# Kernel optimization log

Hardware: AMD Instinct MI355X
Metric: run time of the kernel (lower is better)

Reference implementation:

```python
import jax, jax.numpy as jnp
import numpy as np

F = 64          # n_features
H = F * F       # n_hidden = 4096
P = 4           # proj_size
T = 8192        # timesteps


def _proj_lstm_cell_zero_state(x, W_ih, W_hh, b_ih, b_hh, W_hr):
    """One PyTorch proj-LSTM layer applied per-timestep with zero initial
    (h, c). x: [T, in_dim] -> [T, P].  With h0=0, W_hh contributes 0 and
    f*c_prev vanishes."""
    h0 = jnp.zeros((x.shape[0], W_hh.shape[1]), x.dtype)
    gates = x @ W_ih.T + h0 @ W_hh.T + b_ih + b_hh          # [T, 4H]
    i, f, g, o = jnp.split(gates, 4, axis=-1)               # PyTorch gate order
    c = jax.nn.sigmoid(i) * jnp.tanh(g)                     # f*c0 = 0
    h = jax.nn.sigmoid(o) * jnp.tanh(c)                     # [T, H]
    return h @ W_hr.T                                       # [T, P]


def setup_inputs() -> dict:
    key = jax.random.key(0)
    ks = jax.random.split(key, 17)
    s = 0.05
    d = {"x": jax.random.normal(ks[0], (T, F), jnp.float32)}
    shapes = {
        "W_ih_0": (4 * H, F), "W_hh_0": (4 * H, P), "b_ih_0": (4 * H,),
        "b_hh_0": (4 * H,), "W_hr_0": (P, H),
        "W_ih_1": (4 * H, P), "W_hh_1": (4 * H, P), "b_ih_1": (4 * H,),
        "b_hh_1": (4 * H,), "W_hr_1": (P, H),
        "W_ih_2": (4 * H, P), "W_hh_2": (4 * H, P), "b_ih_2": (4 * H,),
        "b_hh_2": (4 * H,), "W_hr_2": (P, H),
    }
    for i, (name, shp) in enumerate(shapes.items()):
        d[name] = s * jax.random.normal(ks[i + 1], shp, jnp.float32)
    return d


def reference(x,
              W_ih_0, W_hh_0, b_ih_0, b_hh_0, W_hr_0,
              W_ih_1, W_hh_1, b_ih_1, b_hh_1, W_hr_1,
              W_ih_2, W_hh_2, b_ih_2, b_hh_2, W_hr_2):
    # study(): inputs.split(1, dim=0) feeds each timestep as a fresh length-1
    # sequence with zero initial state, so timesteps are independent ->
    # vectorize over T instead of the per-step Python loop.
    h = _proj_lstm_cell_zero_state(x, W_ih_0, W_hh_0, b_ih_0, b_hh_0, W_hr_0)
    h = _proj_lstm_cell_zero_state(h, W_ih_1, W_hh_1, b_ih_1, b_hh_1, W_hr_1)
    h = _proj_lstm_cell_zero_state(h, W_ih_2, W_hh_2, b_ih_2, b_hh_2, W_hr_2)
    return h  # [T, P]
```

## Files before the change

kernel.cpp:

```cpp
#include <hip/hip_runtime.h>

#define TSTEPS 8192
#define HDIM 4096
#define PDIM 4
#define KDIM 64

typedef unsigned short u16;
typedef __attribute__((ext_vector_type(8))) short short8;
typedef __attribute__((ext_vector_type(4))) float f32x4;

#define S1 -1.44269504089f
#define S2 -2.88539008177f

#if __has_builtin(__builtin_amdgcn_exp2f)
#define EXP2(x) __builtin_amdgcn_exp2f(x)
#else
#define EXP2(x) exp2f(x)
#endif
__device__ __forceinline__ float rcpf(float x) { return __builtin_amdgcn_rcpf(x); }

__device__ __forceinline__ void gload16(const void* g, void* l) {
  __builtin_amdgcn_global_load_lds((const __attribute__((address_space(1))) unsigned int*)g,
                                   (__attribute__((address_space(3))) unsigned int*)l,
                                   16, 0, 0);
}

__device__ __forceinline__ u16 bf16_rne(float f) {
  unsigned u = __float_as_uint(f);
  u += 0x7FFF + ((u >> 16) & 1);
  return (u16)(u >> 16);
}
__device__ __forceinline__ void hilo(float v, u16& h, u16& l) {
  h = bf16_rne(v);
  l = bf16_rne(v - __uint_as_float((unsigned)h << 16));
}

#define WS_Y0   0
#define WS_Y1   32768
#define WS_BSC  65536
#define WS_C1   77824
#define WS_C2   159744
#define WS_XHI  241664
#define WS_XLO  503808
#define WS_WHI  765952
#define WS_WLO  1159168
#define WS_PP   1552384

__global__ void prep_kernel(const float* __restrict__ x,
                            const float* __restrict__ Wih0, const float* __restrict__ bih0,
                            const float* __restrict__ bhh0,
                            const float* __restrict__ Wih1, const float* __restrict__ bih1,
                            const float* __restrict__ bhh1, const float* __restrict__ Whr1,
                            const float* __restrict__ Wih2, const float* __restrict__ bih2,
                            const float* __restrict__ bhh2, const float* __restrict__ Whr2,
                            float* __restrict__ ws) {
  const int i = blockIdx.x * 256 + threadIdx.x;
  u16* xhi = (u16*)(ws + WS_XHI);
  u16* xlo = (u16*)(ws + WS_XLO);
  u16* whi = (u16*)(ws + WS_WHI);
  u16* wlo = (u16*)(ws + WS_WLO);

  if (i < 131072) {
    float4 v = *(const float4*)&x[i * 4];
    float val[4] = {v.x, v.y, v.z, v.w};
    u16 h[4], l[4];
#pragma unroll
    for (int e = 0; e < 4; ++e) hilo(val[e], h[e], l[e]);
    *(ushort4*)&xhi[i * 4] = make_ushort4(h[0], h[1], h[2], h[3]);
    *(ushort4*)&xlo[i * 4] = make_ushort4(l[0], l[1], l[2], l[3]);
  } else if (i < 327680) {
    int f = i - 131072;
    int el4 = f * 4;
    int r = el4 >> 6;
    int k4 = el4 & 63;
    int gate = r >> 12, jr = r & 4095;
    int src = (gate == 0) ? jr : (gate + 1) * HDIM + jr;
    float sc = (gate == 1) ? S2 : S1;
    float4 v = *(const float4*)&Wih0[(size_t)src * KDIM + k4];
    float val[4] = {sc * v.x, sc * v.y, sc * v.z, sc * v.w};
    u16 h[4], l[4];
#pragma unroll
    for (int e = 0; e < 4; ++e) hilo(val[e], h[e], l[e]);
    *(ushort4*)&whi[r * KDIM + k4] = make_ushort4(h[0], h[1], h[2], h[3]);
    *(ushort4*)&wlo[r * KDIM + k4] = make_ushort4(l[0], l[1], l[2], l[3]);
  } else if (i < 339968) {
    int f = i - 327680;
    int g = f >> 12, j = f & 4095;
    int src = (g == 0) ? j : (g + 1) * HDIM + j;
    float sc = (g == 1) ? S2 : S1;
    ws[WS_BSC + f] = sc * (bih0[src] + bhh0[src]);
  } else if (i < 348160) {
    int f = i - 339968;
    const float* Wih = (f < 4096) ? Wih1 : Wih2;
    const float* bih = (f < 4096) ? bih1 : bih2;
    const float* bhh = (f < 4096) ? bhh1 : bhh2;
    const float* Whr = (f < 4096) ? Whr1 : Whr2;
    float* c = ws + ((f < 4096) ? WS_C1 : WS_C2);
    int j = f & 4095;
    float4 wi = *(const float4*)&Wih[(size_t)j * 4];
    float4 wg = *(const float4*)&Wih[(size_t)(2 * HDIM + j) * 4];
    float4 wo = *(const float4*)&Wih[(size_t)(3 * HDIM + j) * 4];
    float* cb = c + j * 20;
    *(float4*)(cb + 0)  = make_float4(S1 * wi.x, S1 * wi.y, S1 * wi.z, S1 * wi.w);
    *(float4*)(cb + 4)  = make_float4(S2 * wg.x, S2 * wg.y, S2 * wg.z, S2 * wg.w);
    *(float4*)(cb + 8)  = make_float4(S1 * wo.x, S1 * wo.y, S1 * wo.z, S1 * wo.w);
    *(float4*)(cb + 12) = make_float4(S1 * (bih[j] + bhh[j]),
                                      S2 * (bih[2 * HDIM + j] + bhh[2 * HDIM + j]),
                                      S1 * (bih[3 * HDIM + j] + bhh[3 * HDIM + j]), 0.f);
    *(float4*)(cb + 16) = make_float4(Whr[j], Whr[HDIM + j], Whr[2 * HDIM + j], Whr[3 * HDIM + j]);
  }
}

__global__ __launch_bounds__(256, 2)
void lstm_layer0_mfma(const u16* __restrict__ xhi, const u16* __restrict__ xlo,
                      const u16* __restrict__ whi, const u16* __restrict__ wlo,
                      const float* __restrict__ bsc, const float* __restrict__ Whr,
                      float* __restrict__ pp) {
  __shared__ __align__(16) char smem[65536];
  u16* lx_hi = (u16*)smem;
  u16* lw_hi = (u16*)(smem + 16384);
  u16* lw_lo = (u16*)(smem + 40960);
  float* hsh = (float*)smem;

  const int tid = threadIdx.x;
  const int w = tid >> 6, lane = tid & 63;
  const int m = lane & 15, q = lane >> 4;
  const int jb = blockIdx.x & 63, tb = blockIdx.x >> 6;
  const int j0 = jb * 64;
  const int t0 = tb * 128;

  const int r8 = lane >> 3;
  const int swo = ((lane & 7) ^ r8) * 8;
#pragma unroll
  for (int ui = 0; ui < 16; ++ui) {
    const int u = w * 16 + ui;
    const u16* g;
    char* l;
    if (u < 16) {
      g = xhi + (size_t)(t0 + u * 8 + r8) * 64 + swo;
      l = smem + u * 1024;
    } else if (u < 40) {
      int uu = u - 16;
      g = whi + (size_t)((uu >> 3) * HDIM + j0 + (uu & 7) * 8 + r8) * 64 + swo;
      l = smem + 16384 + uu * 1024;
    } else {
      int uu = u - 40;
      g = wlo + (size_t)((uu >> 3) * HDIM + j0 + (uu & 7) * 8 + r8) * 64 + swo;
      l = smem + 40960 + uu * 1024;
    }
    gload16(g, l);
  }

  f32x4 acc[2][4][3];
#pragma unroll
  for (int ts = 0; ts < 2; ++ts)
#pragma unroll
    for (int js = 0; js < 4; ++js)
#pragma unroll
      for (int g = 0; g < 3; ++g) acc[ts][js][g] = (f32x4){0.f, 0.f, 0.f, 0.f};

  short8 al[2][2];
#pragma unroll
  for (int kc = 0; kc < 2; ++kc)
#pragma unroll
    for (int ts = 0; ts < 2; ++ts)
      al[kc][ts] = *(const short8*)&xlo[(size_t)(t0 + w * 32 + ts * 16 + m) * KDIM + kc * 32 + q * 8];

  __syncthreads();

#pragma unroll
  for (int kc = 0; kc < 2; ++kc) {
    const int cs = ((kc * 4 + q) ^ (m & 7)) * 8;
    short8 ah[2];
#pragma unroll
    for (int ts = 0; ts < 2; ++ts)
      ah[ts] = *(const short8*)&lx_hi[(w * 32 + ts * 16 + m) * 64 + cs];
#pragma unroll
    for (int js = 0; js < 4; ++js) {
#pragma unroll
      for (int g = 0; g < 3; ++g) {
        const int roff = (g * 64 + js * 16 + m) * 64 + cs;
        short8 bh = *(const short8*)&lw_hi[roff];
        short8 bl = *(const short8*)&lw_lo[roff];
#pragma unroll
        for (int ts = 0; ts < 2; ++ts) {
          acc[ts][js][g] = __builtin_amdgcn_mfma_f32_16x16x32_bf16(ah[ts], bh, acc[ts][js][g], 0, 0, 0);
          acc[ts][js][g] = __builtin_amdgcn_mfma_f32_16x16x32_bf16(al[kc][ts], bh, acc[ts][js][g], 0, 0, 0);
          acc[ts][js][g] = __builtin_amdgcn_mfma_f32_16x16x32_bf16(ah[ts], bl, acc[ts][js][g], 0, 0, 0);
        }
      }
    }
  }

  float hreg[2][4][4];
#pragma unroll
  for (int js = 0; js < 4; ++js) {
    const int j = j0 + js * 16 + m;
    float bi = bsc[j];
    float bg = bsc[HDIM + j];
    float bo = bsc[2 * HDIM + j];
#pragma unroll
    for (int ts = 0; ts < 2; ++ts) {
#pragma unroll
      for (int r = 0; r < 4; ++r) {
        float ea = EXP2(acc[ts][js][0][r] + bi);
        float eb = EXP2(acc[ts][js][1][r] + bg);
        float c = (1.0f - eb) * rcpf((1.0f + ea) * (1.0f + eb));
        float ec = EXP2(acc[ts][js][2][r] + bo);
        float ed = EXP2(S2 * c);
        hreg[ts][js][r] = (1.0f - ed) * rcpf((1.0f + ec) * (1.0f + ed));
      }
    }
  }
  __syncthreads();

#pragma unroll
  for (int js = 0; js < 4; ++js)
#pragma unroll
    for (int ts = 0; ts < 2; ++ts)
#pragma unroll
      for (int r = 0; r < 4; ++r)
        hsh[(w * 32 + ts * 16 + q * 4 + r) * 68 + js * 16 + m] = hreg[ts][js][r];
  __syncthreads();

  const int tl = tid & 127;
  const int p0 = (tid >> 7) * 2;
  float s0 = 0.f, s1 = 0.f;
#pragma unroll
  for (int cch = 0; cch < 8; ++cch) {
    const float* wp0 = Whr + (size_t)p0 * HDIM + j0 + cch * 8;
    const float* wp1 = Whr + (size_t)(p0 + 1) * HDIM + j0 + cch * 8;
    float4 w0a = *(const float4*)wp0, w0b = *(const float4*)(wp0 + 4);
    float4 w1a = *(const float4*)wp1, w1b = *(const float4*)(wp1 + 4);
    float4 ha = *(const float4*)&hsh[tl * 68 + cch * 8];
    float4 hb = *(const float4*)&hsh[tl * 68 + cch * 8 + 4];
    float wa[8] = {w0a.x, w0a.y, w0a.z, w0a.w, w0b.x, w0b.y, w0b.z, w0b.w};
    float wb[8] = {w1a.x, w1a.y, w1a.z, w1a.w, w1b.x, w1b.y, w1b.z, w1b.w};
    float hv[8] = {ha.x, ha.y, ha.z, ha.w, hb.x, hb.y, hb.z, hb.w};
#pragma unroll
    for (int e = 0; e < 8; ++e) {
      s0 = fmaf(hv[e], wa[e], s0);
      s1 = fmaf(hv[e], wb[e], s1);
    }
  }
  const int tg = tb * 128 + tl;
  float2 st = {s0, s1};
  *(float2*)&pp[((size_t)jb * TSTEPS + tg) * PDIM + p0] = st;
}

__global__ void reduce64(const float* __restrict__ pp, float* __restrict__ y) {
  const int i = blockIdx.x * 256 + threadIdx.x;
  float s = 0.f;
#pragma unroll 16
  for (int k = 0; k < 64; ++k) s += pp[(size_t)k * (TSTEPS * PDIM) + i];
  y[i] = s;
}

__global__ __launch_bounds__(256, 4)
void lstm_small(const float* __restrict__ xin, const float* __restrict__ cpk,
                float* __restrict__ pp) {
  __shared__ __align__(16) float rec[1280];
  const int tid = threadIdx.x;
  const int tc = blockIdx.x >> 6;
  const int jsp = blockIdx.x & 63;
  const int j0 = jsp * 64;

  for (int i = tid; i < 320; i += 256)
    ((float4*)rec)[i] = ((const float4*)(cpk + (size_t)j0 * 20))[i];

  const int ta = tc * 512 + tid;
  const int tb2 = ta + 256;
  float4 xa = ((const float4*)xin)[ta];
  float4 xb = ((const float4*)xin)[tb2];
  float a0 = 0.f, a1 = 0.f, a2 = 0.f, a3 = 0.f;
  float b0 = 0.f, b1 = 0.f, b2 = 0.f, b3 = 0.f;
  __syncthreads();

#pragma unroll 4
  for (int jj = 0; jj < 64; ++jj) {
    const float* cb = rec + jj * 20;
    float4 wi = *(const float4*)(cb + 0);
    float4 wg = *(const float4*)(cb + 4);
    float4 wo = *(const float4*)(cb + 8);
    float4 bb = *(const float4*)(cb + 12);
    float4 wr = *(const float4*)(cb + 16);
    float gi = bb.x, gg = bb.y, go = bb.z;
    gi = fmaf(xa.x, wi.x, gi); gi = fmaf(xa.y, wi.y, gi);
    gi = fmaf(xa.z, wi.z, gi); gi = fmaf(xa.w, wi.w, gi);
    gg = fmaf(xa.x, wg.x, gg); gg = fmaf(xa.y, wg.y, gg);
    gg = fmaf(xa.z, wg.z, gg); gg = fmaf(xa.w, wg.w, gg);
    go = fmaf(xa.x, wo.x, go); go = fmaf(xa.y, wo.y, go);
    go = fmaf(xa.z, wo.z, go); go = fmaf(xa.w, wo.w, go);
    float ea = EXP2(gi), eb = EXP2(gg);
    float c = (1.0f - eb) * rcpf((1.0f + ea) * (1.0f + eb));
    float ec = EXP2(go), ed = EXP2(S2 * c);
    float h = (1.0f - ed) * rcpf((1.0f + ec) * (1.0f + ed));
    a0 = fmaf(h, wr.x, a0); a1 = fmaf(h, wr.y, a1);
    a2 = fmaf(h, wr.z, a2); a3 = fmaf(h, wr.w, a3);
    gi = bb.x; gg = bb.y; go = bb.z;
    gi = fmaf(xb.x, wi.x, gi); gi = fmaf(xb.y, wi.y, gi);
    gi = fmaf(xb.z, wi.z, gi); gi = fmaf(xb.w, wi.w, gi);
    gg = fmaf(xb.x, wg.x, gg); gg = fmaf(xb.y, wg.y, gg);
    gg = fmaf(xb.z, wg.z, gg); gg = fmaf(xb.w, wg.w, gg);
    go = fmaf(xb.x, wo.x, go); go = fmaf(xb.y, wo.y, go);
    go = fmaf(xb.z, wo.z, go); go = fmaf(xb.w, wo.w, go);
    ea = EXP2(gi); eb = EXP2(gg);
    c = (1.0f - eb) * rcpf((1.0f + ea) * (1.0f + eb));
    ec = EXP2(go); ed = EXP2(S2 * c);
    h = (1.0f - ed) * rcpf((1.0f + ec) * (1.0f + ed));
    b0 = fmaf(h, wr.x, b0); b1 = fmaf(h, wr.y, b1);
    b2 = fmaf(h, wr.z, b2); b3 = fmaf(h, wr.w, b3);
  }

  ((float4*)pp)[(size_t)jsp * TSTEPS + ta]  = make_float4(a0, a1, a2, a3);
  ((float4*)pp)[(size_t)jsp * TSTEPS + tb2] = make_float4(b0, b1, b2, b3);
}

extern "C" void kernel_launch(void* const* d_in, const int* in_sizes, int n_in,
                              void* d_out, int out_size, void* d_ws, size_t ws_size,
                              hipStream_t stream) {
  const float* x    = (const float*)d_in[0];
  const float* Wih0 = (const float*)d_in[1];
  const float* bih0 = (const float*)d_in[3];
  const float* bhh0 = (const float*)d_in[4];
  const float* Whr0 = (const float*)d_in[5];
  const float* Wih1 = (const float*)d_in[6];
  const float* bih1 = (const float*)d_in[8];
  const float* bhh1 = (const float*)d_in[9];
  const float* Whr1 = (const float*)d_in[10];
  const float* Wih2 = (const float*)d_in[11];
  const float* bih2 = (const float*)d_in[13];
  const float* bhh2 = (const float*)d_in[14];
  const float* Whr2 = (const float*)d_in[15];
  float* out = (float*)d_out;
  float* ws = (float*)d_ws;
  float* pp = ws + WS_PP;

  prep_kernel<<<dim3(1360), dim3(256), 0, stream>>>(
      x, Wih0, bih0, bhh0, Wih1, bih1, bhh1, Whr1, Wih2, bih2, bhh2, Whr2, ws);

  lstm_layer0_mfma<<<dim3(4096), dim3(256), 0, stream>>>(
      (const u16*)(ws + WS_XHI), (const u16*)(ws + WS_XLO),
      (const u16*)(ws + WS_WHI), (const u16*)(ws + WS_WLO),
      ws + WS_BSC, Whr0, pp);
  reduce64<<<dim3(128), dim3(256), 0, stream>>>(pp, ws + WS_Y0);

  lstm_small<<<dim3(1024), dim3(256), 0, stream>>>(ws + WS_Y0, ws + WS_C1, pp);
  reduce64<<<dim3(128), dim3(256), 0, stream>>>(pp, ws + WS_Y1);

  lstm_small<<<dim3(1024), dim3(256), 0, stream>>>(ws + WS_Y1, ws + WS_C2, pp);
  reduce64<<<dim3(128), dim3(256), 0, stream>>>(pp, out);
}
```

Measured before the change: 238.4 us.

## Reuse layer-0 weight tiles across two time tiles and shuffle-reduce the projection

The layer-0 MFMA kernel now handles 256 timesteps per block instead of 128. Weight hi/lo tiles stay resident in LDS, and the next x tile is prefetched into LDS while the activations and projection of the first tile run. The projection now uses register-resident Whr and a 16-lane shuffle reduction instead of an LDS round trip of h. Separately, lstm_small drops from two timesteps per thread to one, doubles its grid and raises its occupancy hint. The aim is to halve weight-tile global traffic, shorten the epilogue, and give the small layers more parallelism, at the cost of more registers and shuffles in layer 0.

```diff
diff --git a/kernel.cpp b/kernel.cpp
--- a/kernel.cpp
+++ b/kernel.cpp
@@ -117,135 +117,153 @@
                       const float* __restrict__ bsc, const float* __restrict__ Whr,
                       float* __restrict__ pp) {
   __shared__ __align__(16) char smem[65536];
-  u16* lx_hi = (u16*)smem;
-  u16* lw_hi = (u16*)(smem + 16384);
-  u16* lw_lo = (u16*)(smem + 40960);
-  float* hsh = (float*)smem;
+  u16* lw_hi = (u16*)smem;
+  u16* lw_lo = (u16*)(smem + 24576);
+  u16* lx    = (u16*)(smem + 49152);
 
   const int tid = threadIdx.x;
   const int w = tid >> 6, lane = tid & 63;
   const int m = lane & 15, q = lane >> 4;
-  const int jb = blockIdx.x & 63, tb = blockIdx.x >> 6;
+  const int jb = blockIdx.x & 63, tbb = blockIdx.x >> 6;
   const int j0 = jb * 64;
-  const int t0 = tb * 128;
+  const int t0 = tbb * 256;
 
   const int r8 = lane >> 3;
   const int swo = ((lane & 7) ^ r8) * 8;
+
 #pragma unroll
   for (int ui = 0; ui < 16; ++ui) {
     const int u = w * 16 + ui;
     const u16* g;
     char* l;
-    if (u < 16) {
-      g = xhi + (size_t)(t0 + u * 8 + r8) * 64 + swo;
+    if (u < 24) {
+      g = whi + (size_t)((u >> 3) * HDIM + j0 + (u & 7) * 8 + r8) * 64 + swo;
       l = smem + u * 1024;
-    } else if (u < 40) {
-      int uu = u - 16;
-      g = whi + (size_t)((uu >> 3) * HDIM + j0 + (uu & 7) * 8 + r8) * 64 + swo;
-      l = smem + 16384 + uu * 1024;
+    } else if (u < 48) {
+      int uu = u - 24;
+      g = wlo + (size_t)((uu >> 3) * HDIM + j0 + (uu & 7) * 8 + r8) * 64 + swo;
+      l = smem + 24576 + uu * 1024;
     } else {
-      int uu = u - 40;
-      g = wlo + (size_t)((uu >> 3) * HDIM + j0 + (uu & 7) * 8 + r8) * 64 + swo;
-      l = smem + 40960 + uu * 1024;
+      int uu = u - 48;
+      g = xhi + (size_t)(t0 + uu * 8 + r8) * 64 + swo;
+      l = smem + 49152 + uu * 1024;
     }
     gload16(g, l);
   }
 
+  float whr_v[4][4];
+#pragma unroll
+  for (int p = 0; p < 4; ++p)
+#pragma unroll
+    for (int js = 0; js < 4; ++js)
+      whr_v[p][js] = Whr[(size_t)p * HDIM + j0 + js * 16 + m];
+  float biv[4], bgv[4], bov[4];
+#pragma unroll
+  for (int js = 0; js < 4; ++js) {
+    const int j = j0 + js * 16 + m;
+    biv[js] = bsc[j];
+    bgv[js] = bsc[HDIM + j];
+    bov[js] = bsc[2 * HDIM + j];
+  }
+
   f32x4 acc[2][4][3];
-#pragma unroll
-  for (int ts = 0; ts < 2; ++ts)
-#pragma unroll
-    for (int js = 0; js < 4; ++js)
-#pragma unroll
-      for (int g = 0; g < 3; ++g) acc[ts][js][g] = (f32x4){0.f, 0.f, 0.f, 0.f};
-
   short8 al[2][2];
-#pragma unroll
-  for (int kc = 0; kc < 2; ++kc)
+
+  auto zero_acc = [&]() {
 #pragma unroll
     for (int ts = 0; ts < 2; ++ts)
-      al[kc][ts] = *(const short8*)&xlo[(size_t)(t0 + w * 32 + ts * 16 + m) * KDIM + kc * 32 + q * 8];
-
-  __syncthreads();
-
-#pragma unroll
-  for (int kc = 0; kc < 2; ++kc) {
-    const int cs = ((kc * 4 + q) ^ (m & 7)) * 8;
-    short8 ah[2];
-#pragma unroll
-    for (int ts = 0; ts < 2; ++ts)
-      ah[ts] = *(const short8*)&lx_hi[(w * 32 + ts * 16 + m) * 64 + cs];
-#pragma unroll
-    for (int js = 0; js < 4; ++js) {
-#pragma unroll
-      for (int g = 0; g < 3; ++g) {
-        const int roff = (g * 64 + js * 16 + m) * 64 + cs;
-        short8 bh = *(const short8*)&lw_hi[roff];
-        short8 bl = *(const short8*)&lw_lo[roff];
-#pragma unroll
-        for (int ts = 0; ts < 2; ++ts) {
-          acc[ts][js][g] = __builtin_amdgcn_mfma_f32_16x16x32_bf16(ah[ts], bh, acc[ts][js][g], 0, 0, 0);
-          acc[ts][js][g] = __builtin_amdgcn_mfma_f32_16x16x32_bf16(al[kc][ts], bh, acc[ts][js][g], 0, 0, 0);
-          acc[ts][js][g] = __builtin_amdgcn_mfma_f32_16x16x32_bf16(ah[ts], bl, acc[ts][js][g], 0, 0, 0);
+#pragma unroll
+      for (int js = 0; js < 4; ++js)
+#pragma unroll
+        for (int g = 0; g < 3; ++g) acc[ts][js][g] = (f32x4){0.f, 0.f, 0.f, 0.f};
+  };
+  auto load_al = [&](int tt) {
+#pragma unroll
+    for (int kc = 0; kc < 2; ++kc)
+#pragma unroll
+      for (int ts = 0; ts < 2; ++ts)
+        al[kc][ts] = *(const short8*)&xlo[(size_t)(t0 + tt * 128 + w * 32 + ts * 16 + m) * KDIM + kc * 32 + q * 8];
+  };
+  auto compute = [&]() {
+#pragma unroll
+    for (int kc = 0; kc < 2; ++kc) {
+      const int cs = ((kc * 4 + q) ^ (m & 7)) * 8;
+      short8 ah[2];
+#pragma unroll
+      for (int ts = 0; ts < 2; ++ts)
+        ah[ts] = *(const short8*)&lx[(w * 32 + ts * 16 + m) * 64 + cs];
+#pragma unroll
+      for (int js = 0; js < 4; ++js) {
+#pragma unroll
+        for (int g = 0; g < 3; ++g) {
+          const int roff = (g * 64 + js * 16 + m) * 64 + cs;
+          short8 bh = *(const short8*)&lw_hi[roff];
+          short8 bl = *(const short8*)&lw_lo[roff];
+#pragma unroll
+          for (int ts = 0; ts < 2; ++ts) {
+            acc[ts][js][g] = __builtin_amdgcn_mfma_f32_16x16x32_bf16(ah[ts], bh, acc[ts][js][g], 0, 0, 0);
+            acc[ts][js][g] = __builtin_amdgcn_mfma_f32_16x16x32_bf16(al[kc][ts], bh, acc[ts][js][g], 0, 0, 0);
+            acc[ts][js][g] = __builtin_amdgcn_mfma_f32_16x16x32_bf16(ah[ts], bl, acc[ts][js][g], 0, 0, 0);
+          }
         }
       }
     }
-  }
-
-  float hreg[2][4][4];
-#pragma unroll
-  for (int js = 0; js < 4; ++js) {
-    const int j = j0 + js * 16 + m;
-    float bi = bsc[j];
-    float bg = bsc[HDIM + j];
-    float bo = bsc[2 * HDIM + j];
-#pragma unroll
-    for (int ts = 0; ts < 2; ++ts) {
-#pragma unroll
-      for (int r = 0; r < 4; ++r) {
-        float ea = EXP2(acc[ts][js][0][r] + bi);
-        float eb = EXP2(acc[ts][js][1][r] + bg);
-        float c = (1.0f - eb) * rcpf((1.0f + ea) * (1.0f + eb));
-        float ec = EXP2(acc[ts][js][2][r] + bo);
-        float ed = EXP2(S2 * c);
-        hreg[ts][js][r] = (1.0f - ed) * rcpf((1.0f + ec) * (1.0f + ed));
+  };
+  auto act_proj = [&](int tt) {
+    float hreg[2][4][4];
+#pragma unroll
+    for (int js = 0; js < 4; ++js) {
+#pragma unroll
+      for (int ts = 0; ts < 2; ++ts) {
+#pragma unroll
+        for (int r = 0; r < 4; ++r) {
+          float ea = EXP2(acc[ts][js][0][r] + biv[js]);
+          float eb = EXP2(acc[ts][js][1][r] + bgv[js]);
+          float c = (1.0f - eb) * rcpf((1.0f + ea) * (1.0f + eb));
+          float ec = EXP2(acc[ts][js][2][r] + bov[js]);
+          float ed = EXP2(S2 * c);
+          hreg[ts][js][r] = (1.0f - ed) * rcpf((1.0f + ec) * (1.0f + ed));
+        }
       }
     }
-  }
+#pragma unroll
+    for (int ts = 0; ts < 2; ++ts) {
+#pragma unroll
+      for (int r = 0; r < 4; ++r) {
+        float pv[4];
+#pragma unroll
+        for (int p = 0; p < 4; ++p) {
+          float s = 0.f;
+#pragma unroll
+          for (int js = 0; js < 4; ++js) s = fmaf(hreg[ts][js][r], whr_v[p][js], s);
+#pragma unroll
+          for (int ofs = 1; ofs < 16; ofs <<= 1) s += __shfl_xor(s, ofs, 16);
+          pv[p] = s;
+        }
+        if (m == 0) {
+          const int t = t0 + tt * 128 + w * 32 + ts * 16 + q * 4 + r;
+          *(float4*)&pp[((size_t)jb * TSTEPS + t) * PDIM] = make_float4(pv[0], pv[1], pv[2], pv[3]);
+        }
+      }
+    }
+  };
+
+  load_al(0);
+  zero_acc();
   __syncthreads();
-
-#pragma unroll
-  for (int js = 0; js < 4; ++js)
-#pragma unroll
-    for (int ts = 0; ts < 2; ++ts)
-#pragma unroll
-      for (int r = 0; r < 4; ++r)
-        hsh[(w * 32 + ts * 16 + q * 4 + r) * 68 + js * 16 + m] = hreg[ts][js][r];
+  compute();
   __syncthreads();
-
-  const int tl = tid & 127;
-  const int p0 = (tid >> 7) * 2;
-  float s0 = 0.f, s1 = 0.f;
-#pragma unroll
-  for (int cch = 0; cch < 8; ++cch) {
-    const float* wp0 = Whr + (size_t)p0 * HDIM + j0 + cch * 8;
-    const float* wp1 = Whr + (size_t)(p0 + 1) * HDIM + j0 + cch * 8;
-    float4 w0a = *(const float4*)wp0, w0b = *(const float4*)(wp0 + 4);
-    float4 w1a = *(const float4*)wp1, w1b = *(const float4*)(wp1 + 4);
-    float4 ha = *(const float4*)&hsh[tl * 68 + cch * 8];
-    float4 hb = *(const float4*)&hsh[tl * 68 + cch * 8 + 4];
-    float wa[8] = {w0a.x, w0a.y, w0a.z, w0a.w, w0b.x, w0b.y, w0b.z, w0b.w};
-    float wb[8] = {w1a.x, w1a.y, w1a.z, w1a.w, w1b.x, w1b.y, w1b.z, w1b.w};
-    float hv[8] = {ha.x, ha.y, ha.z, ha.w, hb.x, hb.y, hb.z, hb.w};
-#pragma unroll
-    for (int e = 0; e < 8; ++e) {
-      s0 = fmaf(hv[e], wa[e], s0);
-      s1 = fmaf(hv[e], wb[e], s1);
-    }
-  }
-  const int tg = tb * 128 + tl;
-  float2 st = {s0, s1};
-  *(float2*)&pp[((size_t)jb * TSTEPS + tg) * PDIM + p0] = st;
+#pragma unroll
+  for (int ui = 0; ui < 4; ++ui) {
+    const int u = w * 4 + ui;
+    gload16(xhi + (size_t)(t0 + 128 + u * 8 + r8) * 64 + swo, smem + 49152 + u * 1024);
+  }
+  load_al(1);
+  act_proj(0);
+  zero_acc();
+  __syncthreads();
+  compute();
+  act_proj(1);
 }
 
 __global__ void reduce64(const float* __restrict__ pp, float* __restrict__ y) {
@@ -256,7 +274,7 @@
   y[i] = s;
 }
 
-__global__ __launch_bounds__(256, 4)
+__global__ __launch_bounds__(256, 8)
 void lstm_small(const float* __restrict__ xin, const float* __restrict__ cpk,
                 float* __restrict__ pp) {
   __shared__ __align__(16) float rec[1280];
@@ -268,15 +286,12 @@
   for (int i = tid; i < 320; i += 256)
     ((float4*)rec)[i] = ((const float4*)(cpk + (size_t)j0 * 20))[i];
 
-  const int ta = tc * 512 + tid;
-  const int tb2 = ta + 256;
-  float4 xa = ((const float4*)xin)[ta];
-  float4 xb = ((const float4*)xin)[tb2];
-  float a0 = 0.f, a1 = 0.f, a2 = 0.f, a3 = 0.f;
-  float b0 = 0.f, b1 = 0.f, b2 = 0.f, b3 = 0.f;
+  const int t = tc * 256 + tid;
+  float4 xv = ((const float4*)xin)[t];
+  float o0 = 0.f, o1 = 0.f, o2 = 0.f, o3 = 0.f;
   __syncthreads();
 
-#pragma unroll 4
+#pragma unroll 8
   for (int jj = 0; jj < 64; ++jj) {
     const float* cb = rec + jj * 20;
     float4 wi = *(const float4*)(cb + 0);
@@ -285,35 +300,21 @@
     float4 bb = *(const float4*)(cb + 12);
     float4 wr = *(const float4*)(cb + 16);
     float gi = bb.x, gg = bb.y, go = bb.z;
-    gi = fmaf(xa.x, wi.x, gi); gi = fmaf(xa.y, wi.y, gi);
-    gi = fmaf(xa.z, wi.z, gi); gi = fmaf(xa.w, wi.w, gi);
-    gg = fmaf(xa.x, wg.x, gg); gg = fmaf(xa.y, wg.y, gg);
-    gg = fmaf(xa.z, wg.z, gg); gg = fmaf(xa.w, wg.w, gg);
-    go = fmaf(xa.x, wo.x, go); go = fmaf(xa.y, wo.y, go);
-    go = fmaf(xa.z, wo.z, go); go = fmaf(xa.w, wo.w, go);
+    gi = fmaf(xv.x, wi.x, gi); gi = fmaf(xv.y, wi.y, gi);
+    gi = fmaf(xv.z, wi.z, gi); gi = fmaf(xv.w, wi.w, gi);
+    gg = fmaf(xv.x, wg.x, gg); gg = fmaf(xv.y, wg.y, gg);
+    gg = fmaf(xv.z, wg.z, gg); gg = fmaf(xv.w, wg.w, gg);
+    go = fmaf(xv.x, wo.x, go); go = fmaf(xv.y, wo.y, go);
+    go = fmaf(xv.z, wo.z, go); go = fmaf(xv.w, wo.w, go);
     float ea = EXP2(gi), eb = EXP2(gg);
     float c = (1.0f - eb) * rcpf((1.0f + ea) * (1.0f + eb));
     float ec = EXP2(go), ed = EXP2(S2 * c);
     float h = (1.0f - ed) * rcpf((1.0f + ec) * (1.0f + ed));
-    a0 = fmaf(h, wr.x, a0); a1 = fmaf(h, wr.y, a1);
-    a2 = fmaf(h, wr.z, a2); a3 = fmaf(h, wr.w, a3);
-    gi = bb.x; gg = bb.y; go = bb.z;
-    gi = fmaf(xb.x, wi.x, gi); gi = fmaf(xb.y, wi.y, gi);
-    gi = fmaf(xb.z, wi.z, gi); gi = fmaf(xb.w, wi.w, gi);
-    gg = fmaf(xb.x, wg.x, gg); gg = fmaf(xb.y, wg.y, gg);
-    gg = fmaf(xb.z, wg.z, gg); gg = fmaf(xb.w, wg.w, gg);
-    go = fmaf(xb.x, wo.x, go); go = fmaf(xb.y, wo.y, go);
-    go = fmaf(xb.z, wo.z, go); go = fmaf(xb.w, wo.w, go);
-    ea = EXP2(gi); eb = EXP2(gg);
-    c = (1.0f - eb) * rcpf((1.0f + ea) * (1.0f + eb));
-    ec = EXP2(go); ed = EXP2(S2 * c);
-    h = (1.0f - ed) * rcpf((1.0f + ec) * (1.0f + ed));
-    b0 = fmaf(h, wr.x, b0); b1 = fmaf(h, wr.y, b1);
-    b2 = fmaf(h, wr.z, b2); b3 = fmaf(h, wr.w, b3);
-  }
-
-  ((float4*)pp)[(size_t)jsp * TSTEPS + ta]  = make_float4(a0, a1, a2, a3);
-  ((float4*)pp)[(size_t)jsp * TSTEPS + tb2] = make_float4(b0, b1, b2, b3);
+    o0 = fmaf(h, wr.x, o0); o1 = fmaf(h, wr.y, o1);
+    o2 = fmaf(h, wr.z, o2); o3 = fmaf(h, wr.w, o3);
+  }
+
+  ((float4*)pp)[(size_t)jsp * TSTEPS + t] = make_float4(o0, o1, o2, o3);
 }
 
 extern "C" void kernel_launch(void* const* d_in, const int* in_sizes, int n_in,
@@ -339,15 +340,15 @@
   prep_kernel<<<dim3(1360), dim3(256), 0, stream>>>(
       x, Wih0, bih0, bhh0, Wih1, bih1, bhh1, Whr1, Wih2, bih2, bhh2, Whr2, ws);
 
-  lstm_layer0_mfma<<<dim3(4096), dim3(256), 0, stream>>>(
+  lstm_layer0_mfma<<<dim3(2048), dim3(256), 0, stream>>>(
       (const u16*)(ws + WS_XHI), (const u16*)(ws + WS_XLO),
       (const u16*)(ws + WS_WHI), (const u16*)(ws + WS_WLO),
       ws + WS_BSC, Whr0, pp);
   reduce64<<<dim3(128), dim3(256), 0, stream>>>(pp, ws + WS_Y0);
 
-  lstm_small<<<dim3(1024), dim3(256), 0, stream>>>(ws + WS_Y0, ws + WS_C1, pp);
+  lstm_small<<<dim3(2048), dim3(256), 0, stream>>>(ws + WS_Y0, ws + WS_C1, pp);
   reduce64<<<dim3(128), dim3(256), 0, stream>>>(pp, ws + WS_Y1);
 
-  lstm_small<<<dim3(1024), dim3(256), 0, stream>>>(ws + WS_Y1, ws + WS_C2, pp);
+  lstm_small<<<dim3(2048), dim3(256), 0, stream>>>(ws + WS_Y1, ws + WS_C2, pp);
   reduce64<<<dim3(128), dim3(256), 0, stream>>>(pp, out);
 }
```

Measured after the change: 232.8 us. 1.02x faster.

## Retile layer-0 MFMA kernel, fuse projection via shuffles, use Padé tanh

Applied to the files above, without the earlier changes.

The layer-0 MFMA kernel now handles 64 timesteps per block instead of 128, and each wave covers half of the hidden tile. The x hi/lo fragments load straight from global into registers, and the LDS footprint shrinks so three blocks can fit per CU. The W_hr projection is done in registers with cross-lane shuffle reductions plus a small LDS merge, which replaces the staged h tile and the separate dot-product pass. tanh(c) is replaced everywhere by a rational Padé approximation that saves one exp2. This relies on c staying in (-1,1), and it adds some approximation error and more shuffle work in exchange.

```diff
diff --git a/kernel.cpp b/kernel.cpp
--- a/kernel.cpp
+++ b/kernel.cpp
@@ -18,6 +18,13 @@
 #define EXP2(x) exp2f(x)
 #endif
 __device__ __forceinline__ float rcpf(float x) { return __builtin_amdgcn_rcpf(x); }
+
+__device__ __forceinline__ float h_merge(float c, float ec) {
+  float c2 = c * c;
+  float num = c * fmaf(c2, 10.0f, 105.0f);
+  float den = fmaf(c2, 45.0f, 105.0f) + c2 * c2;
+  return num * rcpf(den * (1.0f + ec));
+}
 
 __device__ __forceinline__ void gload16(const void* g, void* l) {
   __builtin_amdgcn_global_load_lds((const __attribute__((address_space(1))) unsigned int*)g,
@@ -111,141 +118,122 @@
   }
 }
 
-__global__ __launch_bounds__(256, 2)
+__global__ __launch_bounds__(256, 3)
 void lstm_layer0_mfma(const u16* __restrict__ xhi, const u16* __restrict__ xlo,
                       const u16* __restrict__ whi, const u16* __restrict__ wlo,
                       const float* __restrict__ bsc, const float* __restrict__ Whr,
                       float* __restrict__ pp) {
-  __shared__ __align__(16) char smem[65536];
-  u16* lx_hi = (u16*)smem;
-  u16* lw_hi = (u16*)(smem + 16384);
-  u16* lw_lo = (u16*)(smem + 40960);
-  float* hsh = (float*)smem;
+  __shared__ __align__(16) char smem[51200];
+  u16* lw_hi = (u16*)smem;
+  u16* lw_lo = (u16*)(smem + 24576);
+  float* red = (float*)(smem + 49152);
 
   const int tid = threadIdx.x;
   const int w = tid >> 6, lane = tid & 63;
   const int m = lane & 15, q = lane >> 4;
-  const int jb = blockIdx.x & 63, tb = blockIdx.x >> 6;
+  const int th = w & 1, jh = w >> 1;
+  const int jb = blockIdx.x & 63, tbb = blockIdx.x >> 6;
   const int j0 = jb * 64;
-  const int t0 = tb * 128;
-
-  const int r8 = lane >> 3;
-  const int swo = ((lane & 7) ^ r8) * 8;
-#pragma unroll
-  for (int ui = 0; ui < 16; ++ui) {
-    const int u = w * 16 + ui;
+  const int t0 = tbb * 64;
+
+  const int r8_ = lane >> 3;
+  const int swo = ((lane & 7) ^ r8_) * 8;
+
+#pragma unroll
+  for (int ui = 0; ui < 12; ++ui) {
+    const int u = w * 12 + ui;
     const u16* g;
-    char* l;
-    if (u < 16) {
-      g = xhi + (size_t)(t0 + u * 8 + r8) * 64 + swo;
-      l = smem + u * 1024;
-    } else if (u < 40) {
-      int uu = u - 16;
-      g = whi + (size_t)((uu >> 3) * HDIM + j0 + (uu & 7) * 8 + r8) * 64 + swo;
-      l = smem + 16384 + uu * 1024;
+    if (u < 24) {
+      int row = u * 8 + r8_;
+      g = whi + (size_t)((row >> 6) * HDIM + j0 + (row & 63)) * 64 + swo;
     } else {
-      int uu = u - 40;
-      g = wlo + (size_t)((uu >> 3) * HDIM + j0 + (uu & 7) * 8 + r8) * 64 + swo;
-      l = smem + 40960 + uu * 1024;
+      int row = (u - 24) * 8 + r8_;
+      g = wlo + (size_t)((row >> 6) * HDIM + j0 + (row & 63)) * 64 + swo;
     }
-    gload16(g, l);
-  }
-
-  f32x4 acc[2][4][3];
+    gload16(g, smem + u * 1024);
+  }
+
+  short8 ah[2][2], al[2][2];
+#pragma unroll
+  for (int kc = 0; kc < 2; ++kc)
+#pragma unroll
+    for (int ts = 0; ts < 2; ++ts) {
+      size_t ax = (size_t)(t0 + th * 32 + ts * 16 + m) * KDIM + kc * 32 + q * 8;
+      ah[kc][ts] = *(const short8*)&xhi[ax];
+      al[kc][ts] = *(const short8*)&xlo[ax];
+    }
+
+  float whr_v[4][2], biv[2], bgv[2], bov[2];
+#pragma unroll
+  for (int js = 0; js < 2; ++js) {
+    const int j = j0 + jh * 32 + js * 16 + m;
+#pragma unroll
+    for (int p = 0; p < 4; ++p) whr_v[p][js] = Whr[(size_t)p * HDIM + j];
+    biv[js] = bsc[j];
+    bgv[js] = bsc[HDIM + j];
+    bov[js] = bsc[2 * HDIM + j];
+  }
+
+  f32x4 acc[2][2][3];
 #pragma unroll
   for (int ts = 0; ts < 2; ++ts)
 #pragma unroll
-    for (int js = 0; js < 4; ++js)
+    for (int js = 0; js < 2; ++js)
 #pragma unroll
       for (int g = 0; g < 3; ++g) acc[ts][js][g] = (f32x4){0.f, 0.f, 0.f, 0.f};
-
-  short8 al[2][2];
-#pragma unroll
-  for (int kc = 0; kc < 2; ++kc)
-#pragma unroll
-    for (int ts = 0; ts < 2; ++ts)
-      al[kc][ts] = *(const short8*)&xlo[(size_t)(t0 + w * 32 + ts * 16 + m) * KDIM + kc * 32 + q * 8];
 
   __syncthreads();
 
 #pragma unroll
   for (int kc = 0; kc < 2; ++kc) {
     const int cs = ((kc * 4 + q) ^ (m & 7)) * 8;
-    short8 ah[2];
-#pragma unroll
-    for (int ts = 0; ts < 2; ++ts)
-      ah[ts] = *(const short8*)&lx_hi[(w * 32 + ts * 16 + m) * 64 + cs];
-#pragma unroll
-    for (int js = 0; js < 4; ++js) {
+#pragma unroll
+    for (int js = 0; js < 2; ++js) {
 #pragma unroll
       for (int g = 0; g < 3; ++g) {
-        const int roff = (g * 64 + js * 16 + m) * 64 + cs;
+        const int roff = (g * 64 + jh * 32 + js * 16 + m) * 64 + cs;
         short8 bh = *(const short8*)&lw_hi[roff];
         short8 bl = *(const short8*)&lw_lo[roff];
 #pragma unroll
         for (int ts = 0; ts < 2; ++ts) {
-          acc[ts][js][g] = __builtin_amdgcn_mfma_f32_16x16x32_bf16(ah[ts], bh, acc[ts][js][g], 0, 0, 0);
+          acc[ts][js][g] = __builtin_amdgcn_mfma_f32_16x16x32_bf16(ah[kc][ts], bh, acc[ts][js][g], 0, 0, 0);
           acc[ts][js][g] = __builtin_amdgcn_mfma_f32_16x16x32_bf16(al[kc][ts], bh, acc[ts][js][g], 0, 0, 0);
-          acc[ts][js][g] = __builtin_amdgcn_mfma_f32_16x16x32_bf16(ah[ts], bl, acc[ts][js][g], 0, 0, 0);
+          acc[ts][js][g] = __builtin_amdgcn_mfma_f32_16x16x32_bf16(ah[kc][ts], bl, acc[ts][js][g], 0, 0, 0);
         }
       }
     }
   }
 
-  float hreg[2][4][4];
-#pragma unroll
-  for (int js = 0; js < 4; ++js) {
-    const int j = j0 + js * 16 + m;
-    float bi = bsc[j];
-    float bg = bsc[HDIM + j];
-    float bo = bsc[2 * HDIM + j];
-#pragma unroll
-    for (int ts = 0; ts < 2; ++ts) {
-#pragma unroll
-      for (int r = 0; r < 4; ++r) {
-        float ea = EXP2(acc[ts][js][0][r] + bi);
-        float eb = EXP2(acc[ts][js][1][r] + bg);
+#pragma unroll
+  for (int ts = 0; ts < 2; ++ts) {
+#pragma unroll
+    for (int r = 0; r < 4; ++r) {
+      float pv[4] = {0.f, 0.f, 0.f, 0.f};
+#pragma unroll
+      for (int js = 0; js < 2; ++js) {
+        float ea = EXP2(acc[0 * 2 + ts >= 2 ? 1 : ts][js][0][r] + biv[js]);
+        float eb = EXP2(acc[ts][js][1][r] + bgv[js]);
         float c = (1.0f - eb) * rcpf((1.0f + ea) * (1.0f + eb));
-        float ec = EXP2(acc[ts][js][2][r] + bo);
-        float ed = EXP2(S2 * c);
-        hreg[ts][js][r] = (1.0f - ed) * rcpf((1.0f + ec) * (1.0f + ed));
+        float ec = EXP2(acc[ts][js][2][r] + bov[js]);
+        float h = h_merge(c, ec);
+#pragma unroll
+        for (int p = 0; p < 4; ++p) pv[p] = fmaf(h, whr_v[p][js], pv[p]);
+      }
+#pragma unroll
+      for (int p = 0; p < 4; ++p) {
+#pragma unroll
+        for (int ofs = 1; ofs < 16; ofs <<= 1) pv[p] += __shfl_xor(pv[p], ofs, 16);
+      }
+      if (m == 0) {
+        const int tl = th * 32 + ts * 16 + q * 4 + r;
+        *(float4*)&red[(jh * 64 + tl) * 4] = make_float4(pv[0], pv[1], pv[2], pv[3]);
       }
     }
   }
   __syncthreads();
 
-#pragma unroll
-  for (int js = 0; js < 4; ++js)
-#pragma unroll
-    for (int ts = 0; ts < 2; ++ts)
-#pragma unroll
-      for (int r = 0; r < 4; ++r)
-        hsh[(w * 32 + ts * 16 + q * 4 + r) * 68 + js * 16 + m] = hreg[ts][js][r];
-  __syncthreads();
-
-  const int tl = tid & 127;
-  const int p0 = (tid >> 7) * 2;
-  float s0 = 0.f, s1 = 0.f;
-#pragma unroll
-  for (int cch = 0; cch < 8; ++cch) {
-    const float* wp0 = Whr + (size_t)p0 * HDIM + j0 + cch * 8;
-    const float* wp1 = Whr + (size_t)(p0 + 1) * HDIM + j0 + cch * 8;
-    float4 w0a = *(const float4*)wp0, w0b = *(const float4*)(wp0 + 4);
-    float4 w1a = *(const float4*)wp1, w1b = *(const float4*)(wp1 + 4);
-    float4 ha = *(const float4*)&hsh[tl * 68 + cch * 8];
-    float4 hb = *(const float4*)&hsh[tl * 68 + cch * 8 + 4];
-    float wa[8] = {w0a.x, w0a.y, w0a.z, w0a.w, w0b.x, w0b.y, w0b.z, w0b.w};
-    float wb[8] = {w1a.x, w1a.y, w1a.z, w1a.w, w1b.x, w1b.y, w1b.z, w1b.w};
-    float hv[8] = {ha.x, ha.y, ha.z, ha.w, hb.x, hb.y, hb.z, hb.w};
-#pragma unroll
-    for (int e = 0; e < 8; ++e) {
-      s0 = fmaf(hv[e], wa[e], s0);
-      s1 = fmaf(hv[e], wb[e], s1);
-    }
-  }
-  const int tg = tb * 128 + tl;
-  float2 st = {s0, s1};
-  *(float2*)&pp[((size_t)jb * TSTEPS + tg) * PDIM + p0] = st;
+  float s = red[tid] + red[256 + tid];
+  pp[(size_t)jb * (TSTEPS * PDIM) + t0 * PDIM + tid] = s;
 }
 
 __global__ void reduce64(const float* __restrict__ pp, float* __restrict__ y) {
@@ -293,8 +281,7 @@
     go = fmaf(xa.z, wo.z, go); go = fmaf(xa.w, wo.w, go);
     float ea = EXP2(gi), eb = EXP2(gg);
     float c = (1.0f - eb) * rcpf((1.0f + ea) * (1.0f + eb));
-    float ec = EXP2(go), ed = EXP2(S2 * c);
-    float h = (1.0f - ed) * rcpf((1.0f + ec) * (1.0f + ed));
+    float h = h_merge(c, EXP2(go));
     a0 = fmaf(h, wr.x, a0); a1 = fmaf(h, wr.y, a1);
     a2 = fmaf(h, wr.z, a2); a3 = fmaf(h, wr.w, a3);
     gi = bb.x; gg = bb.y; go = bb.z;
@@ -306,8 +293,7 @@
     go = fmaf(xb.z, wo.z, go); go = fmaf(xb.w, wo.w, go);
     ea = EXP2(gi); eb = EXP2(gg);
     c = (1.0f - eb) * rcpf((1.0f + ea) * (1.0f + eb));
-    ec = EXP2(go); ed = EXP2(S2 * c);
-    h = (1.0f - ed) * rcpf((1.0f + ec) * (1.0f + ed));
+    h = h_merge(c, EXP2(go));
     b0 = fmaf(h, wr.x, b0); b1 = fmaf(h, wr.y, b1);
     b2 = fmaf(h, wr.z, b2); b3 = fmaf(h, wr.w, b3);
   }
@@ -339,7 +325,7 @@
   prep_kernel<<<dim3(1360), dim3(256), 0, stream>>>(
       x, Wih0, bih0, bhh0, Wih1, bih1, bhh1, Whr1, Wih2, bih2, bhh2, Whr2, ws);
 
-  lstm_layer0_mfma<<<dim3(4096), dim3(256), 0, stream>>>(
+  lstm_layer0_mfma<<<dim3(8192), dim3(256), 0, stream>>>(
       (const u16*)(ws + WS_XHI), (const u16*)(ws + WS_XLO),
       (const u16*)(ws + WS_WHI), (const u16*)(ws + WS_WLO),
       ws + WS_BSC, Whr0, pp);
```

Result: slower. 251.5 us (+5.5%).
